# Performance work log

Measured on AMD Instinct MI355X. Metric: run time of the kernel, lower is better.

## Reference

```python
import jax, jax.numpy as jnp
import numpy as np

IN_C = 256
OUT_C = 256
KQ_C = 256
HEADS = 8

def setup_inputs() -> dict:
    key = jax.random.key(0)
    kx, kq, kk, kv = jax.random.split(key, 4)
    N, T = 4, 2048
    x = jax.random.normal(kx, (N, IN_C, T), dtype=jnp.float32)
    # Conv1d(kernel_size=1, bias=False) weights: [out, in]
    s = 1.0 / np.sqrt(IN_C)
    Wq = jax.random.uniform(kq, (KQ_C, IN_C), dtype=jnp.float32, minval=-s, maxval=s)
    Wk = jax.random.uniform(kk, (KQ_C, IN_C), dtype=jnp.float32, minval=-s, maxval=s)
    Wv = jax.random.uniform(kv, (OUT_C, IN_C), dtype=jnp.float32, minval=-s, maxval=s)
    return {"x": x, "Wq": Wq, "Wk": Wk, "Wv": Wv}

def reference(x, Wq, Wk, Wv):
    N, C, T = x.shape
    H = HEADS
    dk = KQ_C // H   # head dim for q/k
    dv = OUT_C // H  # head dim for v
    # 1x1 conv == channel matmul: [N,C,T] -> [N,out,T]
    q = jnp.einsum('oc,nct->not', Wq, x).reshape(N, H, dk, T)
    k = jnp.einsum('oc,nct->not', Wk, x).reshape(N, H, dk, T)
    v = jnp.einsum('oc,nct->not', Wv, x).reshape(N, H, dv, T)
    # scores: [N,H,T,T] = q^T k, scaled
    scores = jnp.einsum('nhdt,nhds->nhts', q, k) / np.sqrt(dk).astype(jnp.float32)
    attn = jax.nn.softmax(scores, axis=-1)
    # out: [N,H,T,dv] -> [N,H,dv,T] -> [N,OUT_C,T]
    out = jnp.einsum('nhts,nhds->nhdt', attn, v)
    return out.reshape(N, OUT_C, T)
```

## Files before the change

kernel.cpp:

```cpp
#include <hip/hip_runtime.h>


typedef float f32x4 __attribute__((ext_vector_type(4)));
typedef short short8 __attribute__((ext_vector_type(8)));
typedef short short4v __attribute__((ext_vector_type(4)));

#define WS_Q 0u
#define WS_K (4u << 20)
#define WS_V (8u << 20)
#define WS_X (12u << 20)
#define WS_W (16u << 20)

__device__ __forceinline__ unsigned short f2bf(float f) {
  unsigned int u = __builtin_bit_cast(unsigned int, f);
  u += 0x7FFFu + ((u >> 16) & 1u);
  return (unsigned short)(u >> 16);
}

__device__ __forceinline__ int pack_bf16rn(float a, float b) {
  unsigned int ua = __builtin_bit_cast(unsigned int, a) + 0x8000u;
  unsigned int ub = __builtin_bit_cast(unsigned int, b) + 0x8000u;
  return __builtin_amdgcn_perm(ub, ua, 0x07060302);
}

__global__ __launch_bounds__(256) void pack_kernel(
    const float* __restrict__ x, const float* __restrict__ Wq,
    const float* __restrict__ Wk, const float* __restrict__ Wv,
    unsigned short* __restrict__ ws) {
  const int tid = threadIdx.x;
  const int lane = tid & 63;
  const int wv = tid >> 6;
  const int lc = lane & 15, lq = lane >> 4;
  const int b = blockIdx.x;
  alignas(16) unsigned short tmp[8];
  if (b < 1024) {
    const int r = b * 4 + wv;
    const int kc = r & 7, tt = (r >> 3) & 127, n = r >> 10;
    const int t = tt * 16 + lc;
    const int c0 = kc * 32 + lq * 8;
    const float* src = x + (size_t)(n * 256 + c0) * 2048 + t;
#pragma unroll
    for (int j = 0; j < 8; ++j) tmp[j] = f2bf(src[(size_t)j * 2048]);
    unsigned short* dst = ws + (WS_X >> 1) + (size_t)r * 512 + lane * 8;
    *(int4*)dst = *(const int4*)tmp;
  } else {
    const int r = (b - 1024) * 4 + wv;
    const int kc = r & 7, ot = (r >> 3) & 15, wi = r >> 7;
    const float* W = (wi == 0) ? Wq : (wi == 1) ? Wk : Wv;
    const float scale = (wi == 0) ? 0.25503492f : 1.0f;
    const int o = ot * 16 + lc;
    const int c0 = kc * 32 + lq * 8;
    const float* src = W + o * 256 + c0;
#pragma unroll
    for (int j = 0; j < 8; ++j) tmp[j] = f2bf(src[j] * scale);
    unsigned short* dst = ws + (WS_W >> 1) + (size_t)r * 512 + lane * 8;
    *(int4*)dst = *(const int4*)tmp;
  }
}

__global__ __launch_bounds__(256) void proj_kernel(unsigned short* __restrict__ ws) {
  __shared__ unsigned short eps[4][2048];
  const int tid = threadIdx.x, lane = tid & 63, w = tid >> 6;
  const int lc = lane & 15, lq = lane >> 4;
  const int tt2 = blockIdx.x;
  const int n = blockIdx.y;
  const int wi = blockIdx.z;
  const unsigned short* Xb = ws + (WS_X >> 1);
  const unsigned short* Wb = ws + (WS_W >> 1);

  short8 af[2][8];
#pragma unroll
  for (int mt = 0; mt < 2; ++mt)
#pragma unroll
    for (int kc = 0; kc < 8; ++kc)
      af[mt][kc] = *(const short8*)(Xb + ((size_t)((n * 128 + tt2 * 2 + mt) * 8 + kc) * 512 + lane * 8));

  f32x4 acc[2][4];
#pragma unroll
  for (int mt = 0; mt < 2; ++mt)
#pragma unroll
    for (int nt = 0; nt < 4; ++nt) {
      f32x4 z = {0.f, 0.f, 0.f, 0.f};
      acc[mt][nt] = z;
    }

#pragma unroll
  for (int kc = 0; kc < 8; ++kc) {
    short8 bf[4];
#pragma unroll
    for (int nt = 0; nt < 4; ++nt)
      bf[nt] = *(const short8*)(Wb + ((size_t)((wi * 16 + w * 4 + nt) * 8 + kc) * 512 + lane * 8));
#pragma unroll
    for (int mt = 0; mt < 2; ++mt)
#pragma unroll
      for (int nt = 0; nt < 4; ++nt)
        acc[mt][nt] = __builtin_amdgcn_mfma_f32_16x16x32_bf16(af[mt][kc], bf[nt], acc[mt][nt], 0, 0, 0);
  }

  if (wi < 2) {
    unsigned short* ep = eps[w];
#pragma unroll
    for (int mt = 0; mt < 2; ++mt)
#pragma unroll
      for (int nt = 0; nt < 4; ++nt) {
        const int m2 = ((nt & 1) << 1) | (lc >> 3);
        const int base = ((mt * 2 + (nt >> 1)) << 9) + (m2 << 7) + (lq << 5) + (lc & 7);
#pragma unroll
        for (int r = 0; r < 4; ++r)
          ep[base + ((r ^ m2) << 3)] = f2bf(acc[mt][nt][r]);
      }
    const int swzl = lane ^ (lane >> 4);
    unsigned short* dst = ws + ((wi == 0) ? (WS_Q >> 1) : (WS_K >> 1));
#pragma unroll
    for (int rl = 0; rl < 4; ++rl) {
      int4 v = *(const int4*)(ep + (rl << 9) + swzl * 8);
      const int mt = rl >> 1, hh = rl & 1;
      const int nh = n * 8 + w * 2 + hh;
      const int ttg = tt2 * 2 + mt;
      *(int4*)(dst + ((size_t)(nh * 128 + ttg) * 64 + lane) * 8) = v;
    }
  } else {
    const int kb = tt2 >> 1, sbp = tt2 & 1;
#pragma unroll
    for (int nt = 0; nt < 4; ++nt) {
      const int nh = n * 8 + w * 2 + (nt >> 1);
      const int dt = nt & 1;
      alignas(16) unsigned short tmp[8];
#pragma unroll
      for (int mt = 0; mt < 2; ++mt)
#pragma unroll
        for (int r = 0; r < 4; ++r) tmp[mt * 4 + r] = f2bf(acc[mt][nt][r]);
      unsigned short* dstv = ws + (WS_V >> 1) +
          ((size_t)((((nh * 32 + kb) * 2 + dt) * 2 + sbp)) * 64 + lane) * 8;
      *(int4*)dstv = *(const int4*)tmp;
    }
  }
}

__global__ __launch_bounds__(256) void attn_kernel(const unsigned short* __restrict__ ws,
                                                   float* __restrict__ out) {
  __shared__ __align__(16) char smem[16384];
  const int tid = threadIdx.x, lane = tid & 63, w = tid >> 6;
  const int lc = lane & 15, quad = lane >> 4;
  const int qt = blockIdx.x;
  const int nh = blockIdx.y;

  const unsigned short* Qw = ws + (WS_Q >> 1) + ((size_t)(nh * 128 + qt * 8 + w * 2)) * 512;
  const char* Kp = (const char*)ws + WS_K + (size_t)nh * 131072;
  const char* Vp = (const char*)ws + WS_V + (size_t)nh * 131072;

  short8 qf[2];
  qf[0] = *(const short8*)(Qw + lane * 8);
  qf[1] = *(const short8*)(Qw + 512 + lane * 8);

  *(int4*)(smem + tid * 16) = *(const int4*)(Kp + tid * 16);
  *(int4*)(smem + 4096 + tid * 16) = *(const int4*)(Vp + tid * 16);
  __syncthreads();

  f32x4 acc[2][2];
#pragma unroll
  for (int mt = 0; mt < 2; ++mt)
#pragma unroll
    for (int dt = 0; dt < 2; ++dt) {
      f32x4 z = {0.f, 0.f, 0.f, 0.f};
      acc[mt][dt] = z;
    }
  float lsum[2] = {0.f, 0.f};

  for (int it = 0; it < 32; ++it) {
    int4 pk, pv;
    const bool pre = (it + 1 < 32);
    if (pre) {
      pk = *(const int4*)(Kp + (it + 1) * 4096 + tid * 16);
      pv = *(const int4*)(Vp + (it + 1) * 4096 + tid * 16);
    }
    const unsigned short* kb = (const unsigned short*)(smem + (it & 1) * 8192);
    const unsigned short* vb = kb + 2048;

    short8 kf[4];
#pragma unroll
    for (int sb = 0; sb < 4; ++sb) kf[sb] = *(const short8*)(kb + sb * 512 + lane * 8);
    f32x4 st[2][4];
#pragma unroll
    for (int mt = 0; mt < 2; ++mt)
#pragma unroll
      for (int sb = 0; sb < 4; ++sb) {
        f32x4 z = {0.f, 0.f, 0.f, 0.f};
        st[mt][sb] = __builtin_amdgcn_mfma_f32_16x16x32_bf16(kf[sb], qf[mt], z, 0, 0, 0);
      }

    short4v pf[2][4];
#pragma unroll
    for (int mt = 0; mt < 2; ++mt)
#pragma unroll
      for (int sb = 0; sb < 4; ++sb) {
        float p0 = __builtin_amdgcn_exp2f(st[mt][sb][0]);
        float p1 = __builtin_amdgcn_exp2f(st[mt][sb][1]);
        float p2 = __builtin_amdgcn_exp2f(st[mt][sb][2]);
        float p3 = __builtin_amdgcn_exp2f(st[mt][sb][3]);
        lsum[mt] += (p0 + p1) + (p2 + p3);
        int2 pi;
        pi.x = pack_bf16rn(p0, p1);
        pi.y = pack_bf16rn(p2, p3);
        pf[mt][sb] = __builtin_bit_cast(short4v, pi);
      }

    short4v vf[4][2];
#pragma unroll
    for (int dt = 0; dt < 2; ++dt)
#pragma unroll
      for (int sbp = 0; sbp < 2; ++sbp) {
        short8 vv = *(const short8*)(vb + ((dt * 2 + sbp) * 64 + lane) * 8);
        vf[sbp * 2 + 0][dt] = __builtin_shufflevector(vv, vv, 0, 1, 2, 3);
        vf[sbp * 2 + 1][dt] = __builtin_shufflevector(vv, vv, 4, 5, 6, 7);
      }
#pragma unroll
    for (int sb = 0; sb < 4; ++sb)
#pragma unroll
      for (int mt = 0; mt < 2; ++mt) {
        acc[mt][0] = __builtin_amdgcn_mfma_f32_16x16x16bf16_1k(pf[mt][sb], vf[sb][0], acc[mt][0], 0, 0, 0);
        acc[mt][1] = __builtin_amdgcn_mfma_f32_16x16x16bf16_1k(pf[mt][sb], vf[sb][1], acc[mt][1], 0, 0, 0);
      }

    if (pre) {
      char* db = smem + ((it + 1) & 1) * 8192;
      *(int4*)(db + tid * 16) = pk;
      *(int4*)(db + 4096 + tid * 16) = pv;
    }
    __syncthreads();
  }

  const int chbase = (nh >> 3) * 256 + (nh & 7) * 32;
#pragma unroll
  for (int mt = 0; mt < 2; ++mt) {
    lsum[mt] += __shfl_xor(lsum[mt], 16);
    lsum[mt] += __shfl_xor(lsum[mt], 32);
  }
#pragma unroll
  for (int mt = 0; mt < 2; ++mt) {
    float is[4];
#pragma unroll
    for (int r = 0; r < 4; ++r) is[r] = 1.0f / __shfl(lsum[mt], quad * 4 + r);
    const int tbase = qt * 128 + w * 32 + mt * 16 + quad * 4;
#pragma unroll
    for (int dt = 0; dt < 2; ++dt) {
      float4 ov;
      ov.x = acc[mt][dt][0] * is[0];
      ov.y = acc[mt][dt][1] * is[1];
      ov.z = acc[mt][dt][2] * is[2];
      ov.w = acc[mt][dt][3] * is[3];
      *(float4*)(out + (size_t)(chbase + dt * 16 + lc) * 2048 + tbase) = ov;
    }
  }
}

extern "C" void kernel_launch(void* const* d_in, const int* in_sizes, int n_in,
                              void* d_out, int out_size, void* d_ws, size_t ws_size,
                              hipStream_t stream) {
  const float* x = (const float*)d_in[0];
  const float* Wq = (const float*)d_in[1];
  const float* Wk = (const float*)d_in[2];
  const float* Wv = (const float*)d_in[3];
  unsigned short* ws = (unsigned short*)d_ws;
  float* out = (float*)d_out;
  (void)in_sizes; (void)n_in; (void)out_size; (void)ws_size;

  pack_kernel<<<1120, 256, 0, stream>>>(x, Wq, Wk, Wv, ws);
  proj_kernel<<<dim3(64, 4, 3), 256, 0, stream>>>(ws);
  attn_kernel<<<dim3(16, 32), 256, 0, stream>>>(ws, out);
}
```

Baseline: 114.4 us.

## Split attention over key blocks with partial outputs and a finalize reduction

```diff
diff --git a/kernel.cpp b/kernel.cpp
--- a/kernel.cpp
+++ b/kernel.cpp
@@ -10,6 +10,7 @@
 #define WS_V (8u << 20)
 #define WS_X (12u << 20)
 #define WS_W (16u << 20)
+#define WS_OP (20u << 20)
 
 __device__ __forceinline__ unsigned short f2bf(float f) {
   unsigned int u = __builtin_bit_cast(unsigned int, f);
@@ -137,26 +138,27 @@
   }
 }
 
-__global__ __launch_bounds__(256) void attn_kernel(const unsigned short* __restrict__ ws,
-                                                   float* __restrict__ out) {
-  __shared__ __align__(16) char smem[16384];
-  const int tid = threadIdx.x, lane = tid & 63, w = tid >> 6;
+template <int KS>
+__global__ __launch_bounds__(128, 5) void attn_kernel(
+    const unsigned short* __restrict__ ws, float* __restrict__ out,
+    float* __restrict__ opart, float* __restrict__ lpart) {
+  const int tid = threadIdx.x;
+  const int lane = tid & 63, wv = tid >> 6;
   const int lc = lane & 15, quad = lane >> 4;
-  const int qt = blockIdx.x;
+  const int qw = blockIdx.x * 2 + wv;
   const int nh = blockIdx.y;
-
-  const unsigned short* Qw = ws + (WS_Q >> 1) + ((size_t)(nh * 128 + qt * 8 + w * 2)) * 512;
-  const char* Kp = (const char*)ws + WS_K + (size_t)nh * 131072;
-  const char* Vp = (const char*)ws + WS_V + (size_t)nh * 131072;
+  const int ks = blockIdx.z;
+  constexpr int NKB = 32 / KS;
+  const int kb0 = ks * NKB;
+
+  const unsigned short* Qw = ws + (WS_Q >> 1) + ((size_t)(nh * 128 + qw * 2)) * 512;
+  const unsigned short* Kb = ws + (WS_K >> 1) + (size_t)nh * 65536;
+  const unsigned short* Vb = ws + (WS_V >> 1) + (size_t)nh * 65536;
 
   short8 qf[2];
   qf[0] = *(const short8*)(Qw + lane * 8);
   qf[1] = *(const short8*)(Qw + 512 + lane * 8);
 
-  *(int4*)(smem + tid * 16) = *(const int4*)(Kp + tid * 16);
-  *(int4*)(smem + 4096 + tid * 16) = *(const int4*)(Vp + tid * 16);
-  __syncthreads();
-
   f32x4 acc[2][2];
 #pragma unroll
   for (int mt = 0; mt < 2; ++mt)
@@ -167,52 +169,46 @@
     }
   float lsum[2] = {0.f, 0.f};
 
-  for (int it = 0; it < 32; ++it) {
-    int4 pk, pv;
-    const bool pre = (it + 1 < 32);
-    if (pre) {
-      pk = *(const int4*)(Kp + (it + 1) * 4096 + tid * 16);
-      pv = *(const int4*)(Vp + (it + 1) * 4096 + tid * 16);
-    }
-    const unsigned short* kb = (const unsigned short*)(smem + (it & 1) * 8192);
-    const unsigned short* vb = kb + 2048;
-
-    short8 kf[4];
-#pragma unroll
-    for (int sb = 0; sb < 4; ++sb) kf[sb] = *(const short8*)(kb + sb * 512 + lane * 8);
-    f32x4 st[2][4];
-#pragma unroll
-    for (int mt = 0; mt < 2; ++mt)
+  for (int kb = kb0; kb < kb0 + NKB; ++kb) {
+    const unsigned short* kp = Kb + (size_t)kb * 2048 + lane * 8;
+    const unsigned short* vp = Vb + (size_t)kb * 2048 + lane * 8;
+    short8 kf[4], vv[4];
+#pragma unroll
+    for (int sb = 0; sb < 4; ++sb) kf[sb] = *(const short8*)(kp + sb * 512);
+#pragma unroll
+    for (int u = 0; u < 4; ++u) vv[u] = *(const short8*)(vp + u * 512);
+
+    short4v pf[2][4];
+#pragma unroll
+    for (int mt = 0; mt < 2; ++mt) {
+      f32x4 st[4];
 #pragma unroll
       for (int sb = 0; sb < 4; ++sb) {
         f32x4 z = {0.f, 0.f, 0.f, 0.f};
-        st[mt][sb] = __builtin_amdgcn_mfma_f32_16x16x32_bf16(kf[sb], qf[mt], z, 0, 0, 0);
-      }
-
-    short4v pf[2][4];
-#pragma unroll
-    for (int mt = 0; mt < 2; ++mt)
+        st[sb] = __builtin_amdgcn_mfma_f32_16x16x32_bf16(kf[sb], qf[mt], z, 0, 0, 0);
+      }
 #pragma unroll
       for (int sb = 0; sb < 4; ++sb) {
-        float p0 = __builtin_amdgcn_exp2f(st[mt][sb][0]);
-        float p1 = __builtin_amdgcn_exp2f(st[mt][sb][1]);
-        float p2 = __builtin_amdgcn_exp2f(st[mt][sb][2]);
-        float p3 = __builtin_amdgcn_exp2f(st[mt][sb][3]);
+        float p0 = __builtin_amdgcn_exp2f(st[sb][0]);
+        float p1 = __builtin_amdgcn_exp2f(st[sb][1]);
+        float p2 = __builtin_amdgcn_exp2f(st[sb][2]);
+        float p3 = __builtin_amdgcn_exp2f(st[sb][3]);
         lsum[mt] += (p0 + p1) + (p2 + p3);
         int2 pi;
         pi.x = pack_bf16rn(p0, p1);
         pi.y = pack_bf16rn(p2, p3);
         pf[mt][sb] = __builtin_bit_cast(short4v, pi);
       }
+    }
 
     short4v vf[4][2];
 #pragma unroll
     for (int dt = 0; dt < 2; ++dt)
 #pragma unroll
       for (int sbp = 0; sbp < 2; ++sbp) {
-        short8 vv = *(const short8*)(vb + ((dt * 2 + sbp) * 64 + lane) * 8);
-        vf[sbp * 2 + 0][dt] = __builtin_shufflevector(vv, vv, 0, 1, 2, 3);
-        vf[sbp * 2 + 1][dt] = __builtin_shufflevector(vv, vv, 4, 5, 6, 7);
+        short8 t = vv[dt * 2 + sbp];
+        vf[sbp * 2 + 0][dt] = __builtin_shufflevector(t, t, 0, 1, 2, 3);
+        vf[sbp * 2 + 1][dt] = __builtin_shufflevector(t, t, 4, 5, 6, 7);
       }
 #pragma unroll
     for (int sb = 0; sb < 4; ++sb)
@@ -221,37 +217,64 @@
         acc[mt][0] = __builtin_amdgcn_mfma_f32_16x16x16bf16_1k(pf[mt][sb], vf[sb][0], acc[mt][0], 0, 0, 0);
         acc[mt][1] = __builtin_amdgcn_mfma_f32_16x16x16bf16_1k(pf[mt][sb], vf[sb][1], acc[mt][1], 0, 0, 0);
       }
-
-    if (pre) {
-      char* db = smem + ((it + 1) & 1) * 8192;
-      *(int4*)(db + tid * 16) = pk;
-      *(int4*)(db + 4096 + tid * 16) = pv;
-    }
-    __syncthreads();
-  }
-
-  const int chbase = (nh >> 3) * 256 + (nh & 7) * 32;
+  }
+
 #pragma unroll
   for (int mt = 0; mt < 2; ++mt) {
     lsum[mt] += __shfl_xor(lsum[mt], 16);
     lsum[mt] += __shfl_xor(lsum[mt], 32);
   }
-#pragma unroll
-  for (int mt = 0; mt < 2; ++mt) {
-    float is[4];
-#pragma unroll
-    for (int r = 0; r < 4; ++r) is[r] = 1.0f / __shfl(lsum[mt], quad * 4 + r);
-    const int tbase = qt * 128 + w * 32 + mt * 16 + quad * 4;
-#pragma unroll
-    for (int dt = 0; dt < 2; ++dt) {
-      float4 ov;
-      ov.x = acc[mt][dt][0] * is[0];
-      ov.y = acc[mt][dt][1] * is[1];
-      ov.z = acc[mt][dt][2] * is[2];
-      ov.w = acc[mt][dt][3] * is[3];
-      *(float4*)(out + (size_t)(chbase + dt * 16 + lc) * 2048 + tbase) = ov;
-    }
-  }
+
+  if constexpr (KS == 1) {
+    const int chbase = (nh >> 3) * 256 + (nh & 7) * 32;
+#pragma unroll
+    for (int mt = 0; mt < 2; ++mt) {
+      float is[4];
+#pragma unroll
+      for (int r = 0; r < 4; ++r) is[r] = 1.0f / __shfl(lsum[mt], quad * 4 + r);
+      const int tb = qw * 32 + mt * 16 + quad * 4;
+#pragma unroll
+      for (int dt = 0; dt < 2; ++dt) {
+        f32x4 ov;
+#pragma unroll
+        for (int r = 0; r < 4; ++r) ov[r] = acc[mt][dt][r] * is[r];
+        *(f32x4*)(out + (size_t)(chbase + dt * 16 + lc) * 2048 + tb) = ov;
+      }
+    }
+  } else {
+    const size_t ob = (size_t)(ks * 32 + nh) * 32 * 2048;
+#pragma unroll
+    for (int mt = 0; mt < 2; ++mt) {
+      const int tb = qw * 32 + mt * 16 + quad * 4;
+#pragma unroll
+      for (int dt = 0; dt < 2; ++dt)
+        *(f32x4*)(opart + ob + (size_t)(dt * 16 + lc) * 2048 + tb) = acc[mt][dt];
+      if (quad == 0)
+        lpart[(size_t)(ks * 32 + nh) * 2048 + qw * 32 + mt * 16 + lc] = lsum[mt];
+    }
+  }
+}
+
+template <int KS>
+__global__ __launch_bounds__(256) void finalize_kernel(
+    const float* __restrict__ opart, const float* __restrict__ lpart,
+    float* __restrict__ out) {
+  const int f = blockIdx.x * 256 + threadIdx.x;
+  const int t4 = f & 511;
+  const int c = f >> 9;
+  const int n = c >> 8, ch = c & 255;
+  const int nh = n * 8 + (ch >> 5), d = ch & 31;
+  float4 o = {0.f, 0.f, 0.f, 0.f}, l = {0.f, 0.f, 0.f, 0.f};
+#pragma unroll
+  for (int ks = 0; ks < KS; ++ks) {
+    const float4 ov = *(const float4*)(opart + ((size_t)(ks * 32 + nh) * 32 + d) * 2048 + t4 * 4);
+    const float4 lv = *(const float4*)(lpart + (size_t)(ks * 32 + nh) * 2048 + t4 * 4);
+    o.x += ov.x; o.y += ov.y; o.z += ov.z; o.w += ov.w;
+    l.x += lv.x; l.y += lv.y; l.z += lv.z; l.w += lv.w;
+  }
+  float4 r;
+  r.x = o.x / l.x; r.y = o.y / l.y; r.z = o.z / l.z; r.w = o.w / l.w;
+  *(float4*)(out + (size_t)f * 4) = r;
 }
 
 extern "C" void kernel_launch(void* const* d_in, const int* in_sizes, int n_in,
@@ -263,9 +286,22 @@
   const float* Wv = (const float*)d_in[3];
   unsigned short* ws = (unsigned short*)d_ws;
   float* out = (float*)d_out;
-  (void)in_sizes; (void)n_in; (void)out_size; (void)ws_size;
+  (void)in_sizes; (void)n_in; (void)out_size;
 
   pack_kernel<<<1120, 256, 0, stream>>>(x, Wq, Wk, Wv, ws);
   proj_kernel<<<dim3(64, 4, 3), 256, 0, stream>>>(ws);
-  attn_kernel<<<dim3(16, 32), 256, 0, stream>>>(ws, out);
-}
+
+  char* wsb = (char*)d_ws;
+  float* opart = (float*)(wsb + WS_OP);
+  if (ws_size >= ((size_t)54u << 20)) {
+    float* lpart = (float*)(wsb + WS_OP + ((size_t)4 * 8u << 20));
+    attn_kernel<4><<<dim3(32, 32, 4), 128, 0, stream>>>(ws, out, opart, lpart);
+    finalize_kernel<4><<<2048, 256, 0, stream>>>(opart, lpart, out);
+  } else if (ws_size >= ((size_t)38u << 20)) {
+    float* lpart = (float*)(wsb + WS_OP + ((size_t)2 * 8u << 20));
+    attn_kernel<2><<<dim3(32, 32, 2), 128, 0, stream>>>(ws, out, opart, lpart);
+    finalize_kernel<2><<<2048, 256, 0, stream>>>(opart, lpart, out);
+  } else {
+    attn_kernel<1><<<dim3(32, 32, 1), 128, 0, stream>>>(ws, out, nullptr, nullptr);
+  }
+}
```

Result: faster. 111.7 us (-2.4%).
